# Kernel optimization log

Hardware: AMD Instinct MI355X
Metric: run time of the kernel (lower is better)

Reference implementation:

```python
import jax, jax.numpy as jnp
import numpy as np

WINDOW = 25          # window_size -> h = w = 25, n = 625 tokens
DIM = 512
DIM_HEAD = 64
HEADS = DIM // DIM_HEAD
BATCH = 64


def _rel_pos_indices(ws):
    # mirrors the torch buffer: pairwise relative offsets on a ws x ws grid
    pos = np.arange(ws)
    gi, gj = np.meshgrid(pos, pos, indexing='ij')
    grid = np.stack([gi.reshape(-1), gj.reshape(-1)], axis=-1)      # (ws*ws, 2)
    rel = grid[:, None, :] - grid[None, :, :] + (ws - 1)            # (n, n, 2)
    return (rel[..., 0] * (2 * ws - 1) + rel[..., 1]).astype(np.int32)


def setup_inputs() -> dict:
    key = jax.random.key(0)
    k1, k2, k3, k4 = jax.random.split(key, 4)
    x = jax.random.normal(k1, (BATCH, DIM, WINDOW, WINDOW), jnp.float32)
    w_qkv = jax.random.normal(k2, (DIM, 3 * DIM), jnp.float32) * 0.02   # to_qkv weight (x @ w_qkv)
    w_out = jax.random.normal(k3, (DIM, DIM), jnp.float32) * 0.02       # to_out weight
    rel_pos_bias = jax.random.normal(k4, ((2 * WINDOW - 1) ** 2, HEADS), jnp.float32) * 0.02
    rel_pos_indices = jnp.asarray(_rel_pos_indices(WINDOW))
    return {"x": x, "w_qkv": w_qkv, "w_out": w_out,
            "rel_pos_bias": rel_pos_bias, "rel_pos_indices": rel_pos_indices}


def reference(x, w_qkv, w_out, rel_pos_bias, rel_pos_indices):
    b, d, h, w = x.shape
    n = h * w
    dh = DIM_HEAD
    m = d // dh
    scale = dh ** -0.5
    tokens = x.reshape(b, d, n).transpose(0, 2, 1)                  # b n d
    qkv = tokens @ w_qkv                                            # b n 3d
    q, k, v = jnp.split(qkv, 3, axis=-1)
    split_heads = lambda t: t.reshape(b, n, m, dh).transpose(0, 2, 1, 3)  # b m n dh
    q = split_heads(q) * scale
    k = split_heads(k)
    v = split_heads(v)
    sim = jnp.einsum('bmid,bmjd->bmij', q, k)                       # b m n n
    bias = rel_pos_bias[rel_pos_indices]                            # n n m  (embedding lookup)
    sim = sim + bias.transpose(2, 0, 1)[None]                       # add rel-pos bias inline
    attn = jax.nn.softmax(sim, axis=-1)
    out = jnp.einsum('bmij,bmjd->bmid', attn, v)                    # b m n dh
    out = out.transpose(0, 2, 1, 3).reshape(b, n, m * dh)           # concat heads
    out = out @ w_out                                               # b n d
    return out.transpose(0, 2, 1).reshape(b, d, h, w)
```

## Files before the change

### kernel.cpp

```cpp
#include <hip/hip_runtime.h>
#include <cstdint>
#include <cstddef>

typedef unsigned short u16;
typedef __attribute__((ext_vector_type(8))) short bf16x8;
typedef __attribute__((ext_vector_type(4))) float f32x4;

#define NB    64
#define NTOK  625
#define NTOKP 640
#define DDIM  512
#define NH    8
#define DH    64

__device__ __forceinline__ float bf2f(u16 v) {
    return __uint_as_float(((unsigned int)v) << 16);
}
__device__ __forceinline__ u16 f2bf(float f) {
    unsigned int x = __float_as_uint(f);
    unsigned int r = (x + 0x7fffu + ((x >> 16) & 1u)) >> 16;
    return (u16)r;
}
__device__ __forceinline__ u16 f2bf_fast(float f) {
    return (u16)((__float_as_uint(f) + 0x8000u) >> 16);
}

#if __has_builtin(__builtin_amdgcn_global_load_lds)
typedef const __attribute__((address_space(1))) void gas_void;
typedef __attribute__((address_space(3))) void las_void;
__device__ __forceinline__ void glds16(const void* g, void* l) {
    __builtin_amdgcn_global_load_lds((gas_void*)g, (las_void*)l, 16, 0, 0);
}
#else
__device__ __forceinline__ void glds16(const void* g, void* l) {
    *(uint4*)l = *(const uint4*)g;
}
#endif

__global__ __launch_bounds__(256) void k_transpose_x(const float* __restrict__ x,
                                                     u16* __restrict__ tokens) {
    __shared__ u16 T[64][66];
    int b = blockIdx.z, ct = blockIdx.y, it = blockIdx.x;
    int t = threadIdx.x;
    int i0 = it * 64, c0 = ct * 64;
#pragma unroll
    for (int r = 0; r < 2; r++) {
        int c = (t >> 3) + r * 32;
        int i8 = (t & 7) * 8;
        const float* s = x + ((size_t)b * DDIM + c0 + c) * NTOK + i0 + i8;
#pragma unroll
        for (int u = 0; u < 8; u++)
            T[c][i8 + u] = (i0 + i8 + u < NTOK) ? f2bf(s[u]) : (u16)0;
    }
    __syncthreads();
#pragma unroll
    for (int r = 0; r < 2; r++) {
        int i = (t >> 3) + r * 32;
        int c8 = (t & 7) * 8;
        int gi = i0 + i;
        if (gi < NTOK) {
            u16* d = tokens + ((size_t)b * NTOK + gi) * DDIM + c0 + c8;
#pragma unroll
            for (int u = 0; u < 8; u++) d[u] = T[c8 + u][i];
        }
    }
}

__global__ __launch_bounds__(256) void k_transpose_w(const float* __restrict__ src,
                                                     u16* __restrict__ dst, int R, int C) {
    __shared__ u16 T[64][66];
    int r0 = blockIdx.y * 64, c0 = blockIdx.x * 64;
    int t = threadIdx.x;
#pragma unroll
    for (int rr = 0; rr < 2; rr++) {
        int r = (t >> 3) + rr * 32;
        int c8 = (t & 7) * 8;
        const float* s = src + (size_t)(r0 + r) * C + c0 + c8;
#pragma unroll
        for (int u = 0; u < 8; u++) T[r][c8 + u] = f2bf(s[u]);
    }
    __syncthreads();
#pragma unroll
    for (int rr = 0; rr < 2; rr++) {
        int c = (t >> 3) + rr * 32;
        int r8 = (t & 7) * 8;
        u16* d = dst + (size_t)(c0 + c) * R + r0 + r8;
#pragma unroll
        for (int u = 0; u < 8; u++) d[u] = T[r8 + u][c];
    }
}

__global__ __launch_bounds__(256) void k_bias(const int* __restrict__ rpi,
                                              const float* __restrict__ rpb,
                                              float* __restrict__ biasCf) {
    int blk = blockIdx.x;
    int m = blk / 100, jt = (blk / 10) % 10, it = blk % 10;
    int t = threadIdx.x;
    float vals[16];
#pragma unroll
    for (int jj = 0; jj < 4; jj++) {
        int gj = jt * 64 + jj * 16 + (t & 15);
#pragma unroll
        for (int r = 0; r < 4; r++) {
            int gi = it * 64 + (t >> 6) * 16 + ((t >> 4) & 3) * 4 + r;
            float v;
            if (gj >= NTOK) v = -1e30f;
            else if (gi >= NTOK) v = 0.f;
            else v = rpb[rpi[gi * NTOK + gj] * NH + m];
            vals[jj * 4 + r] = v;
        }
    }
    float* d = biasCf + ((size_t)(m * 10 + jt) * 10 + it) * 4096 + t * 16;
#pragma unroll
    for (int g = 0; g < 4; g++)
        *(f32x4*)(d + g * 4) = *(f32x4*)&vals[g * 4];
}

__global__ __launch_bounds__(256) void k_qkv(const u16* __restrict__ tokens,
                                             const u16* __restrict__ wT,
                                             u16* __restrict__ qk, u16* __restrict__ vT) {
    __shared__ u16 SMEM[16384];
    int bid = blockIdx.x;
    int c8id = bid & 7, t2 = bid >> 3;
    int jt = t2 % 12, q_ = t2 / 12;
    int itb = q_ * 8 + c8id;
    int it = itb % 5, b = itb / 5;
    int i0 = it * 128, j0 = jt * 128;
    int t = threadIdx.x;
    int w = t >> 6, lane = t & 63, quad = lane >> 4, l15 = lane & 15;
    int wr = w >> 1, wc = w & 1;
    f32x4 acc[4][4] = {};
    const u16* abase = tokens + ((size_t)b * NTOK + i0) * DDIM;
    const u16* bbase = wT + (size_t)j0 * DDIM;
    for (int k0 = 0; k0 < DDIM; k0 += 64) {
        __syncthreads();
#pragma unroll
        for (int c = 0; c < 4; c++) {
            int unit = c * 256 + t;
            int row = unit >> 3, cc = unit & 7;
            int gcol = (cc ^ (row & 7)) * 8;
            glds16(abase + (size_t)row * DDIM + k0 + gcol, SMEM + unit * 8);
            glds16(bbase + (size_t)row * DDIM + k0 + gcol, SMEM + 8192 + unit * 8);
        }
        __syncthreads();
#pragma unroll
        for (int kk = 0; kk < 2; kk++) {
            bf16x8 af[4], bfv[4];
            int chA = (((kk * 4 + quad) ^ (l15 & 7))) * 8;
#pragma unroll
            for (int q2 = 0; q2 < 4; q2++) {
                af[q2]  = *(const bf16x8*)&SMEM[(wr * 64 + q2 * 16 + l15) * 64 + chA];
                bfv[q2] = *(const bf16x8*)&SMEM[8192 + (wc * 64 + q2 * 16 + l15) * 64 + chA];
            }
#pragma unroll
            for (int ii = 0; ii < 4; ii++)
#pragma unroll
                for (int jj = 0; jj < 4; jj++)
                    acc[ii][jj] = __builtin_amdgcn_mfma_f32_16x16x32_bf16(af[ii], bfv[jj], acc[ii][jj], 0, 0, 0);
        }
    }
    __syncthreads();
    if (jt < 8) {
        float scale = (j0 < 512) ? 0.125f : 1.0f;
#pragma unroll
        for (int h = 0; h < 2; h++) {
            if (h) __syncthreads();
            if (wr == h) {
#pragma unroll
                for (int ii = 0; ii < 4; ii++)
#pragma unroll
                    for (int jj = 0; jj < 4; jj++)
#pragma unroll
                        for (int r = 0; r < 4; r++)
                            SMEM[(ii * 16 + quad * 4 + r) * 136 + wc * 64 + jj * 16 + l15] =
                                f2bf(acc[ii][jj][r] * scale);
            }
            __syncthreads();
#pragma unroll
            for (int g = 0; g < 4; g++) {
                int unit = g * 256 + t;
                int tok = unit >> 4, ch8 = (unit & 15) * 8;
                int gi = i0 + h * 64 + tok;
                if (gi < NTOK)
                    *(uint4*)(qk + ((size_t)b * NTOK + gi) * 1024 + j0 + ch8) =
                        *(uint4*)&SMEM[tok * 136 + ch8];
            }
        }
    } else {
        int ch0 = j0 - 1024;
#pragma unroll
        for (int h = 0; h < 2; h++) {
            if (h) __syncthreads();
            if (wr == h) {
#pragma unroll
                for (int ii = 0; ii < 4; ii++)
#pragma unroll
                    for (int jj = 0; jj < 4; jj++)
#pragma unroll
                        for (int r = 0; r < 4; r++) {
                            int tok = ii * 16 + quad * 4 + r;
                            int gi = i0 + h * 64 + tok;
                            u16 val = (gi < NTOK) ? f2bf(acc[ii][jj][r]) : (u16)0;
                            SMEM[(wc * 64 + jj * 16 + l15) * 72 + (tok & 15) * 4 + (tok >> 4)] = val;
                        }
            }
            __syncthreads();
#pragma unroll
            for (int g = 0; g < 4; g++) {
                int unit = g * 256 + t;
                int chl = unit >> 3, tok8 = (unit & 7) * 8;
                int chv = ch0 + chl, hd = chv >> 6, tc = chv & 63;
                *(uint4*)(vT + (((size_t)b * NH + hd) * DH + tc) * NTOKP + i0 + h * 64 + tok8) =
                    *(uint4*)&SMEM[chl * 72 + tok8];
            }
        }
    }
}

__global__ __launch_bounds__(256) void k_attn(const u16* __restrict__ qk,
                                              const u16* __restrict__ vT,
                                              const float* __restrict__ biasCf,
                                              u16* __restrict__ attnout) {
    __shared__ u16 Qs[64][72];
    __shared__ u16 Ks[64][72];
    __shared__ u16 Vs[80][72];
    __shared__ u16 Ps[64][72];
    int bid = blockIdx.x;
    int c8id = bid & 7, t2 = bid >> 3;
    int it = t2 % 10, q_ = t2 / 10;
    int bm = q_ * 8 + c8id;
    int m = bm & 7, b = bm >> 3;
    int i0 = it * 64;
    int t = threadIdx.x;
    int w = t >> 6, lane = t & 63, quad = lane >> 4, l15 = lane & 15;
    {
        int row = 64 + (t >> 4), c4 = (t & 15) * 4;
        *(uint2*)&Vs[row][c4] = make_uint2(0x3F803F80u, 0x3F803F80u);
    }
#pragma unroll
    for (int r = 0; r < 2; r++) {
        int row = (t >> 3) + r * 32;
        int t8 = (t & 7) * 8;
        int gi = i0 + row;
        uint4 v;
        if (gi < NTOK) v = *(const uint4*)(qk + ((size_t)b * NTOK + gi) * 1024 + m * DH + t8);
        else v = make_uint4(0, 0, 0, 0);
        *(uint4*)&Qs[row][t8] = v;
    }
    f32x4 oacc[5] = {};
    const u16* vbase = vT + ((size_t)b * NH + m) * DH * NTOKP;
    const float* bC = biasCf + (size_t)(m * 100 + it) * 4096 + t * 16;

    for (int jt = 0; jt < 10; jt++) {
        int j0 = jt * 64;
        __syncthreads();
#pragma unroll
        for (int r = 0; r < 2; r++) {
            int row = (t >> 3) + r * 32;
            int c8 = (t & 7) * 8;
            int gj = j0 + row;
            uint4 kv;
            if (gj < NTOK) kv = *(const uint4*)(qk + ((size_t)b * NTOK + gj) * 1024 + 512 + m * DH + c8);
            else kv = make_uint4(0, 0, 0, 0);
            *(uint4*)&Ks[row][c8] = kv;
            uint4 vv = *(const uint4*)(vbase + (size_t)row * NTOKP + j0 + c8);
            *(uint4*)&Vs[row][c8] = vv;
        }
        __syncthreads();
        const float* bp = bC + (size_t)jt * 10 * 4096;
        f32x4 s[4];
#pragma unroll
        for (int jj = 0; jj < 4; jj++) s[jj] = *(const f32x4*)(bp + jj * 4);
        bf16x8 aq[2];
#pragma unroll
        for (int kk = 0; kk < 2; kk++)
            aq[kk] = *(const bf16x8*)&Qs[w * 16 + l15][kk * 32 + quad * 8];
#pragma unroll
        for (int jj = 0; jj < 4; jj++)
#pragma unroll
            for (int kk = 0; kk < 2; kk++) {
                bf16x8 bk = *(const bf16x8*)&Ks[jj * 16 + l15][kk * 32 + quad * 8];
                s[jj] = __builtin_amdgcn_mfma_f32_16x16x32_bf16(aq[kk], bk, s[jj], 0, 0, 0);
            }
#pragma unroll
        for (int r = 0; r < 4; r++) {
            float p0 = __expf(s[0][r]), p1 = __expf(s[1][r]);
            float p2 = __expf(s[2][r]), p3 = __expf(s[3][r]);
            uint2 pk;
            pk.x = (unsigned)f2bf_fast(p0) | ((unsigned)f2bf_fast(p1) << 16);
            pk.y = (unsigned)f2bf_fast(p2) | ((unsigned)f2bf_fast(p3) << 16);
            *(uint2*)&Ps[w * 16 + quad * 4 + r][l15 * 4] = pk;
        }
        bf16x8 ap[2];
#pragma unroll
        for (int kk = 0; kk < 2; kk++)
            ap[kk] = *(const bf16x8*)&Ps[w * 16 + l15][kk * 32 + quad * 8];
#pragma unroll
        for (int tt = 0; tt < 5; tt++)
#pragma unroll
            for (int kk = 0; kk < 2; kk++) {
                bf16x8 bv = *(const bf16x8*)&Vs[tt * 16 + l15][kk * 32 + quad * 8];
                oacc[tt] = __builtin_amdgcn_mfma_f32_16x16x32_bf16(ap[kk], bv, oacc[tt], 0, 0, 0);
            }
    }
    float rinv[4];
#pragma unroll
    for (int r = 0; r < 4; r++) rinv[r] = __frcp_rn(oacc[4][r]);
#pragma unroll
    for (int tt = 0; tt < 4; tt++)
#pragma unroll
        for (int r = 0; r < 4; r++) {
            int gi = i0 + w * 16 + quad * 4 + r;
            if (gi < NTOK)
                attnout[((size_t)b * NTOK + gi) * DDIM + m * DH + tt * 16 + l15] =
                    f2bf(oacc[tt][r] * rinv[r]);
        }
}

__global__ __launch_bounds__(256) void k_out(const u16* __restrict__ attnout,
                                             const u16* __restrict__ woT,
                                             float* __restrict__ out) {
    __shared__ u16 SMEM[16384];
    int bid = blockIdx.x;
    int c8id = bid & 7, t2 = bid >> 3;
    int jt = t2 % 4, q_ = t2 / 4;
    int itb = q_ * 8 + c8id;
    int it = itb % 5, b = itb / 5;
    int j0 = jt * 128, i0 = it * 128;
    int t = threadIdx.x;
    int w = t >> 6, lane = t & 63, quad = lane >> 4, l15 = lane & 15;
    int wr = w >> 1, wc = w & 1;
    f32x4 acc[4][4] = {};
    const u16* abase = woT + (size_t)j0 * DDIM;
    const u16* bbase = attnout + ((size_t)b * NTOK + i0) * DDIM;
    for (int k0 = 0; k0 < DDIM; k0 += 64) {
        __syncthreads();
#pragma unroll
        for (int c = 0; c < 4; c++) {
            int unit = c * 256 + t;
            int row = unit >> 3, cc = unit & 7;
            int gcol = (cc ^ (row & 7)) * 8;
            glds16(abase + (size_t)row * DDIM + k0 + gcol, SMEM + unit * 8);
            glds16(bbase + (size_t)row * DDIM + k0 + gcol, SMEM + 8192 + unit * 8);
        }
        __syncthreads();
#pragma unroll
        for (int kk = 0; kk < 2; kk++) {
            bf16x8 af[4], bfv[4];
            int chA = (((kk * 4 + quad) ^ (l15 & 7))) * 8;
#pragma unroll
            for (int q2 = 0; q2 < 4; q2++) {
                af[q2]  = *(const bf16x8*)&SMEM[(wr * 64 + q2 * 16 + l15) * 64 + chA];
                bfv[q2] = *(const bf16x8*)&SMEM[8192 + (wc * 64 + q2 * 16 + l15) * 64 + chA];
            }
#pragma unroll
            for (int ii = 0; ii < 4; ii++)
#pragma unroll
                for (int jj = 0; jj < 4; jj++)
                    acc[ii][jj] = __builtin_amdgcn_mfma_f32_16x16x32_bf16(af[ii], bfv[jj], acc[ii][jj], 0, 0, 0);
        }
    }
#pragma unroll
    for (int ii = 0; ii < 4; ii++)
#pragma unroll
        for (int jj = 0; jj < 4; jj++) {
            int gi = i0 + wc * 64 + jj * 16 + l15;
            if (gi >= NTOK) continue;
#pragma unroll
            for (int r = 0; r < 4; r++) {
                int gj = j0 + wr * 64 + ii * 16 + quad * 4 + r;
                out[((size_t)b * DDIM + gj) * NTOK + gi] = acc[ii][jj][r];
            }
        }
}

extern "C" void kernel_launch(void* const* d_in, const int* in_sizes, int n_in,
                              void* d_out, int out_size, void* d_ws, size_t ws_size,
                              hipStream_t stream) {
    const float* x    = (const float*)d_in[0];
    const float* wqkv = (const float*)d_in[1];
    const float* wout = (const float*)d_in[2];
    const float* rpb  = (const float*)d_in[3];
    const int*   rpi  = (const int*)d_in[4];
    float* out = (float*)d_out;

    char* ws = (char*)d_ws;
    size_t off = 0;
    auto alloc = [&](size_t nbytes) -> void* {
        void* p = ws + off;
        off += (nbytes + 255) & ~(size_t)255;
        return p;
    };
    u16* tokens   = (u16*)alloc((size_t)NB * NTOK * DDIM * 2);
    u16* qk       = (u16*)alloc((size_t)NB * NTOK * 1024 * 2);
    u16* vT       = (u16*)alloc((size_t)NB * NH * DH * NTOKP * 2);
    u16* wqkvT    = (u16*)alloc((size_t)1536 * DDIM * 2);
    u16* woutT    = (u16*)alloc((size_t)DDIM * DDIM * 2);
    float* biasCf = (float*)alloc((size_t)NH * 100 * 4096 * 4);
    u16* attnout  = tokens;

    k_transpose_x<<<dim3(10, 8, NB), 256, 0, stream>>>(x, tokens);
    k_transpose_w<<<dim3(1536 / 64, DDIM / 64), 256, 0, stream>>>(wqkv, wqkvT, DDIM, 1536);
    k_transpose_w<<<dim3(DDIM / 64, DDIM / 64), 256, 0, stream>>>(wout, woutT, DDIM, DDIM);
    k_bias<<<dim3(800), 256, 0, stream>>>(rpi, rpb, biasCf);
    k_qkv<<<dim3(3840), 256, 0, stream>>>(tokens, wqkvT, qk, vT);
    k_attn<<<dim3(5120), 256, 0, stream>>>(qk, vT, biasCf, attnout);
    k_out<<<dim3(1280), 256, 0, stream>>>(attnout, woutT, out);
}
```

Before: 508.8 us.

## Pad token buffers to 640 rows and shrink GEMM K-tile for higher occupancy

Token, QK and attention-output buffers are padded to 640 rows per batch, so the guarded loads and stores in the transpose, QKV, attention and output kernels become unconditional. The QKV and output GEMMs move from a 64-wide to a 32-wide K step with a new 4-chunk swizzle. This halves their LDS footprint, and launch bounds now request 4 blocks per CU. The attention kernel hoists the Q fragment load out of the KV loop and computes the row-sum column with a preloaded ones fragment. The cost is twice as many barriers per GEMM, more workspace memory, and reliance on padded rows holding zero or finite values.

```diff
diff --git a/kernel.cpp b/kernel.cpp
--- a/kernel.cpp
+++ b/kernel.cpp
@@ -58,11 +58,9 @@
         int i = (t >> 3) + r * 32;
         int c8 = (t & 7) * 8;
         int gi = i0 + i;
-        if (gi < NTOK) {
-            u16* d = tokens + ((size_t)b * NTOK + gi) * DDIM + c0 + c8;
-#pragma unroll
-            for (int u = 0; u < 8; u++) d[u] = T[c8 + u][i];
-        }
+        u16* d = tokens + ((size_t)b * NTOKP + gi) * DDIM + c0 + c8;
+#pragma unroll
+        for (int u = 0; u < 8; u++) d[u] = T[c8 + u][i];
     }
 }
 
@@ -116,10 +114,10 @@
         *(f32x4*)(d + g * 4) = *(f32x4*)&vals[g * 4];
 }
 
-__global__ __launch_bounds__(256) void k_qkv(const u16* __restrict__ tokens,
-                                             const u16* __restrict__ wT,
-                                             u16* __restrict__ qk, u16* __restrict__ vT) {
-    __shared__ u16 SMEM[16384];
+__global__ __launch_bounds__(256, 4) void k_qkv(const u16* __restrict__ tokens,
+                                                const u16* __restrict__ wT,
+                                                u16* __restrict__ qk, u16* __restrict__ vT) {
+    __shared__ u16 SMEM[9216];
     int bid = blockIdx.x;
     int c8id = bid & 7, t2 = bid >> 3;
     int jt = t2 % 12, q_ = t2 / 12;
@@ -129,35 +127,33 @@
     int t = threadIdx.x;
     int w = t >> 6, lane = t & 63, quad = lane >> 4, l15 = lane & 15;
     int wr = w >> 1, wc = w & 1;
+    int swl = (l15 + (l15 >> 2)) & 3;
     f32x4 acc[4][4] = {};
-    const u16* abase = tokens + ((size_t)b * NTOK + i0) * DDIM;
+    const u16* abase = tokens + ((size_t)b * NTOKP + i0) * DDIM;
     const u16* bbase = wT + (size_t)j0 * DDIM;
-    for (int k0 = 0; k0 < DDIM; k0 += 64) {
-        __syncthreads();
-#pragma unroll
-        for (int c = 0; c < 4; c++) {
+    for (int k0 = 0; k0 < DDIM; k0 += 32) {
+        __syncthreads();
+#pragma unroll
+        for (int c = 0; c < 2; c++) {
             int unit = c * 256 + t;
-            int row = unit >> 3, cc = unit & 7;
-            int gcol = (cc ^ (row & 7)) * 8;
+            int row = unit >> 2, cc = unit & 3;
+            int gcol = (cc ^ ((row + (row >> 2)) & 3)) * 8;
             glds16(abase + (size_t)row * DDIM + k0 + gcol, SMEM + unit * 8);
-            glds16(bbase + (size_t)row * DDIM + k0 + gcol, SMEM + 8192 + unit * 8);
-        }
-        __syncthreads();
-#pragma unroll
-        for (int kk = 0; kk < 2; kk++) {
-            bf16x8 af[4], bfv[4];
-            int chA = (((kk * 4 + quad) ^ (l15 & 7))) * 8;
-#pragma unroll
-            for (int q2 = 0; q2 < 4; q2++) {
-                af[q2]  = *(const bf16x8*)&SMEM[(wr * 64 + q2 * 16 + l15) * 64 + chA];
-                bfv[q2] = *(const bf16x8*)&SMEM[8192 + (wc * 64 + q2 * 16 + l15) * 64 + chA];
-            }
-#pragma unroll
-            for (int ii = 0; ii < 4; ii++)
-#pragma unroll
-                for (int jj = 0; jj < 4; jj++)
-                    acc[ii][jj] = __builtin_amdgcn_mfma_f32_16x16x32_bf16(af[ii], bfv[jj], acc[ii][jj], 0, 0, 0);
-        }
+            glds16(bbase + (size_t)row * DDIM + k0 + gcol, SMEM + 4096 + unit * 8);
+        }
+        __syncthreads();
+        bf16x8 af[4], bfv[4];
+        int chA = (quad ^ swl) * 8;
+#pragma unroll
+        for (int q2 = 0; q2 < 4; q2++) {
+            af[q2]  = *(const bf16x8*)&SMEM[(wr * 64 + q2 * 16 + l15) * 32 + chA];
+            bfv[q2] = *(const bf16x8*)&SMEM[4096 + (wc * 64 + q2 * 16 + l15) * 32 + chA];
+        }
+#pragma unroll
+        for (int ii = 0; ii < 4; ii++)
+#pragma unroll
+            for (int jj = 0; jj < 4; jj++)
+                acc[ii][jj] = __builtin_amdgcn_mfma_f32_16x16x32_bf16(af[ii], bfv[jj], acc[ii][jj], 0, 0, 0);
     }
     __syncthreads();
     if (jt < 8) {
@@ -180,10 +176,8 @@
             for (int g = 0; g < 4; g++) {
                 int unit = g * 256 + t;
                 int tok = unit >> 4, ch8 = (unit & 15) * 8;
-                int gi = i0 + h * 64 + tok;
-                if (gi < NTOK)
-                    *(uint4*)(qk + ((size_t)b * NTOK + gi) * 1024 + j0 + ch8) =
-                        *(uint4*)&SMEM[tok * 136 + ch8];
+                *(uint4*)(qk + ((size_t)b * NTOKP + i0 + h * 64 + tok) * 1024 + j0 + ch8) =
+                    *(uint4*)&SMEM[tok * 136 + ch8];
             }
         }
     } else {
@@ -199,9 +193,8 @@
 #pragma unroll
                         for (int r = 0; r < 4; r++) {
                             int tok = ii * 16 + quad * 4 + r;
-                            int gi = i0 + h * 64 + tok;
-                            u16 val = (gi < NTOK) ? f2bf(acc[ii][jj][r]) : (u16)0;
-                            SMEM[(wc * 64 + jj * 16 + l15) * 72 + (tok & 15) * 4 + (tok >> 4)] = val;
+                            SMEM[(wc * 64 + jj * 16 + l15) * 72 + (tok & 15) * 4 + (tok >> 4)] =
+                                f2bf(acc[ii][jj][r]);
                         }
             }
             __syncthreads();
@@ -241,11 +234,15 @@
     for (int r = 0; r < 2; r++) {
         int row = (t >> 3) + r * 32;
         int t8 = (t & 7) * 8;
-        int gi = i0 + row;
-        uint4 v;
-        if (gi < NTOK) v = *(const uint4*)(qk + ((size_t)b * NTOK + gi) * 1024 + m * DH + t8);
-        else v = make_uint4(0, 0, 0, 0);
-        *(uint4*)&Qs[row][t8] = v;
+        *(uint4*)&Qs[row][t8] =
+            *(const uint4*)(qk + ((size_t)b * NTOKP + i0 + row) * 1024 + m * DH + t8);
+    }
+    __syncthreads();
+    bf16x8 aq[2], vones[2];
+#pragma unroll
+    for (int kk = 0; kk < 2; kk++) {
+        aq[kk]    = *(const bf16x8*)&Qs[w * 16 + l15][kk * 32 + quad * 8];
+        vones[kk] = *(const bf16x8*)&Vs[64 + l15][kk * 32 + quad * 8];
     }
     f32x4 oacc[5] = {};
     const u16* vbase = vT + ((size_t)b * NH + m) * DH * NTOKP;
@@ -258,23 +255,15 @@
         for (int r = 0; r < 2; r++) {
             int row = (t >> 3) + r * 32;
             int c8 = (t & 7) * 8;
-            int gj = j0 + row;
-            uint4 kv;
-            if (gj < NTOK) kv = *(const uint4*)(qk + ((size_t)b * NTOK + gj) * 1024 + 512 + m * DH + c8);
-            else kv = make_uint4(0, 0, 0, 0);
-            *(uint4*)&Ks[row][c8] = kv;
-            uint4 vv = *(const uint4*)(vbase + (size_t)row * NTOKP + j0 + c8);
-            *(uint4*)&Vs[row][c8] = vv;
+            *(uint4*)&Ks[row][c8] =
+                *(const uint4*)(qk + ((size_t)b * NTOKP + j0 + row) * 1024 + 512 + m * DH + c8);
+            *(uint4*)&Vs[row][c8] = *(const uint4*)(vbase + (size_t)row * NTOKP + j0 + c8);
         }
         __syncthreads();
         const float* bp = bC + (size_t)jt * 10 * 4096;
         f32x4 s[4];
 #pragma unroll
         for (int jj = 0; jj < 4; jj++) s[jj] = *(const f32x4*)(bp + jj * 4);
-        bf16x8 aq[2];
-#pragma unroll
-        for (int kk = 0; kk < 2; kk++)
-            aq[kk] = *(const bf16x8*)&Qs[w * 16 + l15][kk * 32 + quad * 8];
 #pragma unroll
         for (int jj = 0; jj < 4; jj++)
 #pragma unroll
@@ -296,12 +285,15 @@
         for (int kk = 0; kk < 2; kk++)
             ap[kk] = *(const bf16x8*)&Ps[w * 16 + l15][kk * 32 + quad * 8];
 #pragma unroll
-        for (int tt = 0; tt < 5; tt++)
+        for (int tt = 0; tt < 4; tt++)
 #pragma unroll
             for (int kk = 0; kk < 2; kk++) {
                 bf16x8 bv = *(const bf16x8*)&Vs[tt * 16 + l15][kk * 32 + quad * 8];
                 oacc[tt] = __builtin_amdgcn_mfma_f32_16x16x32_bf16(ap[kk], bv, oacc[tt], 0, 0, 0);
             }
+#pragma unroll
+        for (int kk = 0; kk < 2; kk++)
+            oacc[4] = __builtin_amdgcn_mfma_f32_16x16x32_bf16(ap[kk], vones[kk], oacc[4], 0, 0, 0);
     }
     float rinv[4];
 #pragma unroll
@@ -312,15 +304,15 @@
         for (int r = 0; r < 4; r++) {
             int gi = i0 + w * 16 + quad * 4 + r;
             if (gi < NTOK)
-                attnout[((size_t)b * NTOK + gi) * DDIM + m * DH + tt * 16 + l15] =
+                attnout[((size_t)b * NTOKP + gi) * DDIM + m * DH + tt * 16 + l15] =
                     f2bf(oacc[tt][r] * rinv[r]);
         }
 }
 
-__global__ __launch_bounds__(256) void k_out(const u16* __restrict__ attnout,
-                                             const u16* __restrict__ woT,
-                                             float* __restrict__ out) {
-    __shared__ u16 SMEM[16384];
+__global__ __launch_bounds__(256, 4) void k_out(const u16* __restrict__ attnout,
+                                                const u16* __restrict__ woT,
+                                                float* __restrict__ out) {
+    __shared__ u16 SMEM[8192];
     int bid = blockIdx.x;
     int c8id = bid & 7, t2 = bid >> 3;
     int jt = t2 % 4, q_ = t2 / 4;
@@ -330,35 +322,33 @@
     int t = threadIdx.x;
     int w = t >> 6, lane = t & 63, quad = lane >> 4, l15 = lane & 15;
     int wr = w >> 1, wc = w & 1;
+    int swl = (l15 + (l15 >> 2)) & 3;
     f32x4 acc[4][4] = {};
     const u16* abase = woT + (size_t)j0 * DDIM;
-    const u16* bbase = attnout + ((size_t)b * NTOK + i0) * DDIM;
-    for (int k0 = 0; k0 < DDIM; k0 += 64) {
-        __syncthreads();
-#pragma unroll
-        for (int c = 0; c < 4; c++) {
+    const u16* bbase = attnout + ((size_t)b * NTOKP + i0) * DDIM;
+    for (int k0 = 0; k0 < DDIM; k0 += 32) {
+        __syncthreads();
+#pragma unroll
+        for (int c = 0; c < 2; c++) {
             int unit = c * 256 + t;
-            int row = unit >> 3, cc = unit & 7;
-            int gcol = (cc ^ (row & 7)) * 8;
+            int row = unit >> 2, cc = unit & 3;
+            int gcol = (cc ^ ((row + (row >> 2)) & 3)) * 8;
             glds16(abase + (size_t)row * DDIM + k0 + gcol, SMEM + unit * 8);
-            glds16(bbase + (size_t)row * DDIM + k0 + gcol, SMEM + 8192 + unit * 8);
-        }
-        __syncthreads();
-#pragma unroll
-        for (int kk = 0; kk < 2; kk++) {
-            bf16x8 af[4], bfv[4];
-            int chA = (((kk * 4 + quad) ^ (l15 & 7))) * 8;
-#pragma unroll
-            for (int q2 = 0; q2 < 4; q2++) {
-                af[q2]  = *(const bf16x8*)&SMEM[(wr * 64 + q2 * 16 + l15) * 64 + chA];
-                bfv[q2] = *(const bf16x8*)&SMEM[8192 + (wc * 64 + q2 * 16 + l15) * 64 + chA];
-            }
-#pragma unroll
-            for (int ii = 0; ii < 4; ii++)
-#pragma unroll
-                for (int jj = 0; jj < 4; jj++)
-                    acc[ii][jj] = __builtin_amdgcn_mfma_f32_16x16x32_bf16(af[ii], bfv[jj], acc[ii][jj], 0, 0, 0);
-        }
+            glds16(bbase + (size_t)row * DDIM + k0 + gcol, SMEM + 4096 + unit * 8);
+        }
+        __syncthreads();
+        bf16x8 af[4], bfv[4];
+        int chA = (quad ^ swl) * 8;
+#pragma unroll
+        for (int q2 = 0; q2 < 4; q2++) {
+            af[q2]  = *(const bf16x8*)&SMEM[(wr * 64 + q2 * 16 + l15) * 32 + chA];
+            bfv[q2] = *(const bf16x8*)&SMEM[4096 + (wc * 64 + q2 * 16 + l15) * 32 + chA];
+        }
+#pragma unroll
+        for (int ii = 0; ii < 4; ii++)
+#pragma unroll
+            for (int jj = 0; jj < 4; jj++)
+                acc[ii][jj] = __builtin_amdgcn_mfma_f32_16x16x32_bf16(af[ii], bfv[jj], acc[ii][jj], 0, 0, 0);
     }
 #pragma unroll
     for (int ii = 0; ii < 4; ii++)
@@ -391,8 +381,8 @@
         off += (nbytes + 255) & ~(size_t)255;
         return p;
     };
-    u16* tokens   = (u16*)alloc((size_t)NB * NTOK * DDIM * 2);
-    u16* qk       = (u16*)alloc((size_t)NB * NTOK * 1024 * 2);
+    u16* tokens   = (u16*)alloc((size_t)NB * NTOKP * DDIM * 2);
+    u16* qk       = (u16*)alloc((size_t)NB * NTOKP * 1024 * 2);
     u16* vT       = (u16*)alloc((size_t)NB * NH * DH * NTOKP * 2);
     u16* wqkvT    = (u16*)alloc((size_t)1536 * DDIM * 2);
     u16* woutT    = (u16*)alloc((size_t)DDIM * DDIM * 2);
```

Measured after the change: 419.5 us. -17.6%, faster.
